# Kernel tuning notes

Measured on AMD Instinct MI355X. Metric: run time of the kernel, lower is better.

The kernel has to match this reference:

```python
import jax, jax.numpy as jnp
import numpy as np

EPS = 1e-5
NHEAD = 8

def layer_norm(x, g, b):
    mu = jnp.mean(x, axis=-1, keepdims=True)
    var = jnp.mean((x - mu) ** 2, axis=-1, keepdims=True)
    return (x - mu) * jax.lax.rsqrt(var + EPS) * g + b

def setup_inputs() -> dict:
    key = jax.random.key(0)
    ks = jax.random.split(key, 8)
    B, S, D, F = 4, 2048, 512, 2048
    s = 0.02
    return {
        "x": jax.random.normal(ks[0], (B, S, D), jnp.float32),
        "Wqkv": jax.random.normal(ks[1], (3 * D, D), jnp.float32) * s,
        "bqkv": jnp.zeros((3 * D,), jnp.float32),
        "Wo": jax.random.normal(ks[2], (D, D), jnp.float32) * s,
        "bo": jnp.zeros((D,), jnp.float32),
        "W1": jax.random.normal(ks[3], (F, D), jnp.float32) * s,
        "b1": jnp.zeros((F,), jnp.float32),
        "W2": jax.random.normal(ks[4], (D, F), jnp.float32) * s,
        "b2": jnp.zeros((D,), jnp.float32),
        "g1": jnp.ones((D,), jnp.float32),
        "bn1": jnp.zeros((D,), jnp.float32),
        "g2": jnp.ones((D,), jnp.float32),
        "bn2": jnp.zeros((D,), jnp.float32),
    }

def reference(x, Wqkv, bqkv, Wo, bo, W1, b1, W2, b2, g1, bn1, g2, bn2):
    B, S, D = x.shape
    H = NHEAD
    hd = D // H
    # fused QKV projection (torch MultiheadAttention in_proj)
    qkv = x @ Wqkv.T + bqkv                      # [B,S,3D]
    q, k, v = jnp.split(qkv, 3, axis=-1)
    q = q.reshape(B, S, H, hd).transpose(0, 2, 1, 3)  # [B,H,S,hd]
    k = k.reshape(B, S, H, hd).transpose(0, 2, 1, 3)
    v = v.reshape(B, S, H, hd).transpose(0, 2, 1, 3)
    scores = jnp.einsum("bhqd,bhkd->bhqk", q, k) / jnp.sqrt(jnp.float32(hd))
    causal = jnp.tril(jnp.ones((S, S), bool))
    scores = jnp.where(causal, scores, jnp.float32(-jnp.inf))
    attn = jax.nn.softmax(scores, axis=-1)
    ctx = jnp.einsum("bhqk,bhkd->bhqd", attn, v)        # [B,H,S,hd]
    ctx = ctx.transpose(0, 2, 1, 3).reshape(B, S, D)
    attn_out = ctx @ Wo.T + bo
    # residual + LayerNorm 1
    x = layer_norm(x + attn_out, g1, bn1)
    # FFN (ReLU) + residual + LayerNorm 2
    ff = jax.nn.relu(x @ W1.T + b1) @ W2.T + b2
    x = layer_norm(x + ff, g2, bn2)
    return x
```

## Files before the change

### kernel.cpp

```cpp
#include <hip/hip_runtime.h>
#include <hip/hip_bf16.h>
#include <math.h>

#define D_MODEL 512
#define SEQ     2048
#define BATCH   4
#define NHEADS  8
#define HDIM    64
#define FFN     2048
#define TOKENS  (BATCH*SEQ)

typedef __attribute__((ext_vector_type(8))) short bf16x8;
typedef __attribute__((ext_vector_type(4))) float f32x4;

__device__ inline ushort f2bf(float f) {
    unsigned u = __builtin_bit_cast(unsigned, f);
    unsigned r = (u + 0x7fffu + ((u >> 16) & 1u)) >> 16;
    return (ushort)r;
}
__device__ inline ushort f2bf_fast(float f) {
    return (ushort)((__builtin_bit_cast(unsigned, f) + 0x8000u) >> 16);
}

#define GLOAD_LDS16(g, l) __builtin_amdgcn_global_load_lds( \
    (const __attribute__((address_space(1))) void*)(g), \
    (__attribute__((address_space(3))) void*)(l), 16, 0, 0)

__global__ void cast_all_bf16(const float* __restrict__ x, const float* __restrict__ Wqkv,
                              const float* __restrict__ Wo, const float* __restrict__ W1,
                              const float* __restrict__ W2, ushort* __restrict__ outbase) {
    const int i = blockIdx.x * blockDim.x + threadIdx.x;
    if (i >= 1835008) return;
    float4 v;
    if      (i < 1048576) v = ((const float4*)x)[i];
    else if (i < 1245184) v = ((const float4*)Wqkv)[i - 1048576];
    else if (i < 1310720) v = ((const float4*)Wo)[i - 1245184];
    else if (i < 1572864) v = ((const float4*)W1)[i - 1310720];
    else                  v = ((const float4*)W2)[i - 1572864];
    ushort4 o;
    o.x = f2bf(v.x); o.y = f2bf(v.y); o.z = f2bf(v.z); o.w = f2bf(v.w);
    ((ushort4*)outbase)[i] = o;
}

template<int MODE, int RELU>
__global__ __launch_bounds__(256) void gemm_bt_mfma(const ushort* __restrict__ A,
                                                    const ushort* __restrict__ W,
                                                    const float* __restrict__ bias,
                                                    void* __restrict__ CoutA,
                                                    void* __restrict__ CoutB,
                                                    ushort* __restrict__ Qc,
                                                    ushort* __restrict__ Kc,
                                                    ushort* __restrict__ Vt,
                                                    int M, int N, int Kstride, int Klen) {
    __shared__ ushort Asb[128 * 32];
    __shared__ ushort Bsb[128 * 32];

    const int tid  = threadIdx.x;
    const int lane = tid & 63;
    const int wv   = tid >> 6;
    const int m0   = blockIdx.y * 128;
    const int n0   = blockIdx.x * 128;
    const int wm   = (wv >> 1) * 64;
    const int wn   = (wv & 1) * 64;
    const int ksel = (MODE == 3) ? blockIdx.z : 0;

    const ushort* Ab = A + (size_t)ksel * Klen;
    const ushort* Wb = W + (size_t)ksel * Klen;

    const int eA = wv * 1024 + lane * 8;
    const int rA = eA >> 5, cA = eA & 31;
    const ushort* gA0 = Ab + (size_t)(m0 + rA) * Kstride + cA;
    const ushort* gA1 = gA0 + (size_t)16 * Kstride;
    const ushort* gB0 = Wb + (size_t)(n0 + rA) * Kstride + cA;
    const ushort* gB1 = gB0 + (size_t)16 * Kstride;
    ushort* lA0 = Asb + wv * 1024;
    ushort* lA1 = Asb + wv * 1024 + 512;
    ushort* lB0 = Bsb + wv * 1024;
    ushort* lB1 = Bsb + wv * 1024 + 512;

    f32x4 acc[4][4] = {};

    const int fr = lane & 15;
    const int fk = (lane >> 4) * 8;

    for (int k0 = 0; k0 < Klen; k0 += 32) {
        GLOAD_LDS16(gA0, lA0); GLOAD_LDS16(gA1, lA1);
        GLOAD_LDS16(gB0, lB0); GLOAD_LDS16(gB1, lB1);
        gA0 += 32; gA1 += 32; gB0 += 32; gB1 += 32;
        __syncthreads();

        bf16x8 af[4], bfr[4];
        #pragma unroll
        for (int i = 0; i < 4; ++i)
            af[i] = *(const bf16x8*)(Asb + (wm + i * 16 + fr) * 32 + fk);
        #pragma unroll
        for (int j = 0; j < 4; ++j)
            bfr[j] = *(const bf16x8*)(Bsb + (wn + j * 16 + fr) * 32 + fk);

        #pragma unroll
        for (int i = 0; i < 4; ++i)
            #pragma unroll
            for (int j = 0; j < 4; ++j)
                acc[i][j] = __builtin_amdgcn_mfma_f32_16x16x32_bf16(af[i], bfr[j], acc[i][j], 0, 0, 0);
        __syncthreads();
    }

    const int col  = lane & 15;
    const int rowq = (lane >> 4) * 4;
    #pragma unroll
    for (int i = 0; i < 4; ++i) {
        const int gm = m0 + wm + i * 16 + rowq;
        #pragma unroll
        for (int j = 0; j < 4; ++j) {
            const int gn = n0 + wn + j * 16 + col;
            if (MODE == 2) {
                const float bv = bias[gn];
                const int seg = gn >> 9;
                const int h   = (gn >> 6) & 7;
                const int dd  = gn & 63;
                const int bb  = gm >> 11;
                const int ss  = gm & 2047;
                const int bh  = bb * 8 + h;
                if (seg == 2) {
                    ushort4 pk;
                    pk.x = f2bf(acc[i][j][0] + bv);
                    pk.y = f2bf(acc[i][j][1] + bv);
                    pk.z = f2bf(acc[i][j][2] + bv);
                    pk.w = f2bf(acc[i][j][3] + bv);
                    *(ushort4*)(Vt + ((size_t)bh * 64 + dd) * 2048 + ss) = pk;
                } else {
                    ushort* dst = (seg == 0 ? Qc : Kc) + ((size_t)bh * 2048 + ss) * 64 + dd;
                    #pragma unroll
                    for (int r = 0; r < 4; ++r)
                        dst[(size_t)r * 64] = f2bf(acc[i][j][r] + bv);
                }
            } else if (MODE == 3) {
                float* dst = (float*)(ksel ? CoutB : CoutA);
                const float bv = ksel ? 0.f : bias[gn];
                #pragma unroll
                for (int r = 0; r < 4; ++r)
                    dst[(size_t)(gm + r) * N + gn] = acc[i][j][r] + bv;
            } else {
                const float bv = bias[gn];
                #pragma unroll
                for (int r = 0; r < 4; ++r) {
                    float v = acc[i][j][r] + bv;
                    if (RELU) v = fmaxf(v, 0.f);
                    ((ushort*)CoutA)[(size_t)(gm + r) * N + gn] = f2bf(v);
                }
            }
        }
    }
}

__device__ __forceinline__ void attn_step(const ushort* __restrict__ Kb,
                                          const ushort* __restrict__ Vb,
                                          ushort* __restrict__ Psw,
                                          bf16x8 qf0, bf16x8 qf1,
                                          float (&lp)[4], f32x4 (&o)[4],
                                          int qw, int j0, bool diag,
                                          int col, int g, int c7) {
    f32x4 s[4] = {};
    #pragma unroll
    for (int nt = 0; nt < 4; ++nt) {
        const int kr = nt * 16 + col;
        bf16x8 kf0 = *(const bf16x8*)(Kb + kr * 64 + (((g    ) ^ c7) * 8));
        bf16x8 kf1 = *(const bf16x8*)(Kb + kr * 64 + (((g + 4) ^ c7) * 8));
        s[nt] = __builtin_amdgcn_mfma_f32_16x16x32_bf16(qf0, kf0, s[nt], 0, 0, 0);
        s[nt] = __builtin_amdgcn_mfma_f32_16x16x32_bf16(qf1, kf1, s[nt], 0, 0, 0);
    }

    if (diag) {
        #pragma unroll
        for (int nt = 0; nt < 4; ++nt)
            #pragma unroll
            for (int r = 0; r < 4; ++r)
                if ((j0 + nt * 16 + col) > (qw + 4 * g + r)) s[nt][r] = -INFINITY;
    }

    #pragma unroll
    for (int nt = 0; nt < 4; ++nt)
        #pragma unroll
        for (int r = 0; r < 4; ++r) {
            float p = __expf(s[nt][r] * 0.125f);
            s[nt][r] = p;
            lp[r] += p;
        }

    #pragma unroll
    for (int nt = 0; nt < 4; ++nt)
        #pragma unroll
        for (int r = 0; r < 4; ++r) {
            const int q  = 4 * g + r;
            const int bc = 32 * nt + 2 * col;
            *(ushort*)((char*)Psw + q * 128 + (((bc >> 4) ^ (q & 7)) * 16) + (bc & 15)) =
                f2bf_fast(s[nt][r]);
        }

    {
        bf16x8 pf0 = *(const bf16x8*)(Psw + col * 64 + (((g    ) ^ c7) * 8));
        bf16x8 pf1 = *(const bf16x8*)(Psw + col * 64 + (((g + 4) ^ c7) * 8));
        #pragma unroll
        for (int nt = 0; nt < 4; ++nt) {
            const int vr = nt * 16 + col;
            bf16x8 vf0 = *(const bf16x8*)(Vb + vr * 64 + (((g    ) ^ c7) * 8));
            bf16x8 vf1 = *(const bf16x8*)(Vb + vr * 64 + (((g + 4) ^ c7) * 8));
            o[nt] = __builtin_amdgcn_mfma_f32_16x16x32_bf16(pf0, vf0, o[nt], 0, 0, 0);
            o[nt] = __builtin_amdgcn_mfma_f32_16x16x32_bf16(pf1, vf1, o[nt], 0, 0, 0);
        }
    }
}

__global__ __launch_bounds__(256) void attn_mfma_kernel(const ushort* __restrict__ Qc,
                                                        const ushort* __restrict__ Kc,
                                                        const ushort* __restrict__ Vt,
                                                        ushort* __restrict__ ctxb) {
    __shared__ ushort Ks[2 * 64 * 64];
    __shared__ ushort Vs[2 * 64 * 64];
    __shared__ ushort Ps[64 * 64];

    const int tid  = threadIdx.x;
    const int lane = tid & 63;
    const int wv   = tid >> 6;
    const int pair = blockIdx.x;
    const int bh   = blockIdx.y;
    const int q0a  = pair * 64;
    const int q0b  = (31 - pair) * 64;
    const int qwA  = q0a + wv * 16;
    const int qwB  = q0b + wv * 16;

    const int col = lane & 15;
    const int g   = lane >> 4;
    const int c7  = col & 7;

    bf16x8 qfA0, qfA1, qfB0, qfB1;
    {
        const ushort* qa = Qc + ((size_t)bh * 2048 + qwA + col) * 64 + g * 8;
        qfA0 = *(const bf16x8*)qa;
        qfA1 = *(const bf16x8*)(qa + 32);
        const ushort* qb = Qc + ((size_t)bh * 2048 + qwB + col) * 64 + g * 8;
        qfB0 = *(const bf16x8*)qb;
        qfB1 = *(const bf16x8*)(qb + 32);
    }

    const int srow = tid >> 2;
    const int sch  = 2 * (tid & 3);
    const ushort* Kg = Kc + ((size_t)bh * 2048 + srow) * 64 + sch * 8;
    const ushort* Vg = Vt + ((size_t)bh * 64 + srow) * 2048 + sch * 8;
    const int ko0 = srow * 64 + (((sch    ) ^ (srow & 7)) * 8);
    const int ko1 = srow * 64 + (((sch + 1) ^ (srow & 7)) * 8);
    ushort* Psw = Ps + wv * 1024;

    float lpa[4] = {}, lpb[4] = {};
    f32x4 oa[4] = {}, ob[4] = {};

    bf16x8 pk0 = *(const bf16x8*)(Kg);
    bf16x8 pk1 = *(const bf16x8*)(Kg + 8);
    bf16x8 pv0 = *(const bf16x8*)(Vg);
    bf16x8 pv1 = *(const bf16x8*)(Vg + 8);

    for (int j0 = 0; j0 <= q0b; j0 += 64) {
        const int par = (j0 >> 6) & 1;
        ushort* Kb = Ks + par * 4096;
        ushort* Vb = Vs + par * 4096;
        *(bf16x8*)(Kb + ko0) = pk0; *(bf16x8*)(Kb + ko1) = pk1;
        *(bf16x8*)(Vb + ko0) = pv0; *(bf16x8*)(Vb + ko1) = pv1;
        __syncthreads();

        if (j0 < q0b) {
            pk0 = *(const bf16x8*)(Kg + (size_t)(j0 + 64) * 64);
            pk1 = *(const bf16x8*)(Kg + (size_t)(j0 + 64) * 64 + 8);
            pv0 = *(const bf16x8*)(Vg + j0 + 64);
            pv1 = *(const bf16x8*)(Vg + j0 + 72);
        }

        if (j0 <= q0a)
            attn_step(Kb, Vb, Psw, qfA0, qfA1, lpa, oa, qwA, j0, j0 == q0a, col, g, c7);
        attn_step(Kb, Vb, Psw, qfB0, qfB1, lpb, ob, qwB, j0, j0 == q0b, col, g, c7);
    }

    const int b = bh >> 3, h = bh & 7;
    #pragma unroll
    for (int r = 0; r < 4; ++r) {
        float la = lpa[r];
        la += __shfl_xor(la, 1); la += __shfl_xor(la, 2);
        la += __shfl_xor(la, 4); la += __shfl_xor(la, 8);
        float lb = lpb[r];
        lb += __shfl_xor(lb, 1); lb += __shfl_xor(lb, 2);
        lb += __shfl_xor(lb, 4); lb += __shfl_xor(lb, 8);
        const float inva = 1.f / la;
        const float invb = 1.f / lb;
        const size_t rowa = ((size_t)b * 2048 + qwA + 4 * g + r) * 512 + h * 64;
        const size_t rowb = ((size_t)b * 2048 + qwB + 4 * g + r) * 512 + h * 64;
        #pragma unroll
        for (int nt = 0; nt < 4; ++nt) {
            ctxb[rowa + nt * 16 + col] = f2bf(oa[nt][r] * inva);
            ctxb[rowb + nt * 16 + col] = f2bf(ob[nt][r] * invb);
        }
    }
}

template<int WRITE_BF16>
__global__ void ln_residual(const float* __restrict__ A, const float* __restrict__ B1,
                            const float* __restrict__ B2,
                            const float* __restrict__ g, const float* __restrict__ beta,
                            float* __restrict__ out, ushort* __restrict__ outb) {
    __shared__ float sbuf[8];
    const int row = blockIdx.x;
    const int tid = threadIdx.x;
    const size_t base = (size_t)row * D_MODEL;

    float v0 = A[base + tid]       + B1[base + tid]       + B2[base + tid];
    float v1 = A[base + tid + 256] + B1[base + tid + 256] + B2[base + tid + 256];

    float sum = v0 + v1;
    #pragma unroll
    for (int off = 32; off; off >>= 1) sum += __shfl_xor(sum, off);
    if ((tid & 63) == 0) sbuf[tid >> 6] = sum;
    __syncthreads();
    if (tid == 0) { float t = 0.f; for (int i = 0; i < 4; ++i) t += sbuf[i]; sbuf[4] = t; }
    __syncthreads();
    const float mu = sbuf[4] * (1.f / 512.f);
    __syncthreads();

    float d0 = v0 - mu, d1 = v1 - mu;
    float sq = d0 * d0 + d1 * d1;
    #pragma unroll
    for (int off = 32; off; off >>= 1) sq += __shfl_xor(sq, off);
    if ((tid & 63) == 0) sbuf[tid >> 6] = sq;
    __syncthreads();
    if (tid == 0) { float t = 0.f; for (int i = 0; i < 4; ++i) t += sbuf[i]; sbuf[4] = t; }
    __syncthreads();
    const float var = sbuf[4] * (1.f / 512.f);
    const float rs  = rsqrtf(var + 1e-5f);

    float r0 = d0 * rs * g[tid]       + beta[tid];
    float r1 = d1 * rs * g[tid + 256] + beta[tid + 256];
    out[base + tid]       = r0;
    out[base + tid + 256] = r1;
    if (WRITE_BF16) {
        outb[base + tid]       = f2bf(r0);
        outb[base + tid + 256] = f2bf(r1);
    }
}

extern "C" void kernel_launch(void* const* d_in, const int* in_sizes, int n_in,
                              void* d_out, int out_size, void* d_ws, size_t ws_size,
                              hipStream_t stream) {
    const float* x    = (const float*)d_in[0];
    const float* Wqkv = (const float*)d_in[1];
    const float* bqkv = (const float*)d_in[2];
    const float* Wo   = (const float*)d_in[3];
    const float* bo   = (const float*)d_in[4];
    const float* W1   = (const float*)d_in[5];
    const float* b1   = (const float*)d_in[6];
    const float* W2   = (const float*)d_in[7];
    const float* b2   = (const float*)d_in[8];
    const float* g1   = (const float*)d_in[9];
    const float* bn1  = (const float*)d_in[10];
    const float* g2   = (const float*)d_in[11];
    const float* bn2  = (const float*)d_in[12];

    float* ws = (float*)d_ws;
    ushort* Qcb     = (ushort*)ws;
    ushort* Kcb     = (ushort*)(ws + 2097152);
    ushort* Vtb     = (ushort*)(ws + 4194304);
    float*  attn_b  = ws;
    ushort* ff1b    = (ushort*)ws;
    float*  ff2a    = ws + 8388608;
    float*  attn_a  = ws + 12582912;
    float*  ff2b    = ws + 12582912;
    float*  ln1     = ws + 16777216;
    ushort* ctxb  = (ushort*)(ws + 20971520);
    ushort* ln1b  = (ushort*)(ws + 23068672);
    ushort* xb    = (ushort*)(ws + 25165824);
    ushort* Wqkvb = (ushort*)(ws + 27262976);
    float*  out   = (float*)d_out;
    ushort* W1b   = (ushort*)(ws + 27787264);
    ushort* W2b   = (ushort*)(ws + 28311552);
    ushort* Wob   = (ushort*)(ws + 27656192);

    const dim3 blk(256);

    cast_all_bf16<<<dim3(7168), blk, 0, stream>>>(x, Wqkv, Wo, W1, W2, xb);

    gemm_bt_mfma<2,0><<<dim3(1536/128, 8192/128), blk, 0, stream>>>(
        xb, Wqkvb, bqkv, nullptr, nullptr, Qcb, Kcb, Vtb, TOKENS, 1536, 512, 512);
    attn_mfma_kernel<<<dim3(16, BATCH*NHEADS), blk, 0, stream>>>(Qcb, Kcb, Vtb, ctxb);
    gemm_bt_mfma<3,0><<<dim3(512/128, 8192/128, 2), blk, 0, stream>>>(
        ctxb, Wob, bo, attn_a, attn_b, nullptr, nullptr, nullptr, TOKENS, 512, 512, 256);
    ln_residual<1><<<dim3(TOKENS), blk, 0, stream>>>(x, attn_a, attn_b, g1, bn1, ln1, ln1b);
    gemm_bt_mfma<1,1><<<dim3(2048/128, 8192/128), blk, 0, stream>>>(
        ln1b, W1b, b1, ff1b, nullptr, nullptr, nullptr, nullptr, TOKENS, 2048, 512, 512);
    gemm_bt_mfma<3,0><<<dim3(512/128, 8192/128, 2), blk, 0, stream>>>(
        ff1b, W2b, b2, ff2a, ff2b, nullptr, nullptr, nullptr, TOKENS, 512, 2048, 1024);
    ln_residual<0><<<dim3(TOKENS), blk, 0, stream>>>(ln1, ff2a, ff2b, g2, bn2, out, nullptr);
}
```

Measured before the change: 269.9 us.

## Split attention key range across two partitions and add a combine kernel

The causal attention kernel now launches a second grid dimension that splits the key tiles between two blocks by even/odd tile index. Each block writes unnormalized fp32 partial outputs and row sums to workspace. A new combine kernel adds the two partials, normalizes, and writes the bf16 context. This doubles the number of blocks to improve latency hiding and CU occupancy, at the cost of extra fp32 partial writes and reads plus one more kernel launch.

```diff
diff --git a/kernel.cpp b/kernel.cpp
--- a/kernel.cpp
+++ b/kernel.cpp
@@ -214,7 +214,8 @@
 __global__ __launch_bounds__(256) void attn_mfma_kernel(const ushort* __restrict__ Qc,
                                                         const ushort* __restrict__ Kc,
                                                         const ushort* __restrict__ Vt,
-                                                        ushort* __restrict__ ctxb) {
+                                                        float* __restrict__ opart,
+                                                        float* __restrict__ lpart) {
     __shared__ ushort Ks[2 * 64 * 64];
     __shared__ ushort Vs[2 * 64 * 64];
     __shared__ ushort Ps[64 * 64];
@@ -224,10 +225,12 @@
     const int wv   = tid >> 6;
     const int pair = blockIdx.x;
     const int bh   = blockIdx.y;
+    const int z    = blockIdx.z;
     const int q0a  = pair * 64;
     const int q0b  = (31 - pair) * 64;
     const int qwA  = q0a + wv * 16;
     const int qwB  = q0b + wv * 16;
+    const int jtmax = 31 - pair;
 
     const int col = lane & 15;
     const int g   = lane >> 4;
@@ -254,24 +257,25 @@
     float lpa[4] = {}, lpb[4] = {};
     f32x4 oa[4] = {}, ob[4] = {};
 
-    bf16x8 pk0 = *(const bf16x8*)(Kg);
-    bf16x8 pk1 = *(const bf16x8*)(Kg + 8);
-    bf16x8 pv0 = *(const bf16x8*)(Vg);
-    bf16x8 pv1 = *(const bf16x8*)(Vg + 8);
-
-    for (int j0 = 0; j0 <= q0b; j0 += 64) {
-        const int par = (j0 >> 6) & 1;
+    bf16x8 pk0 = *(const bf16x8*)(Kg + (size_t)(z << 6) * 64);
+    bf16x8 pk1 = *(const bf16x8*)(Kg + (size_t)(z << 6) * 64 + 8);
+    bf16x8 pv0 = *(const bf16x8*)(Vg + (z << 6));
+    bf16x8 pv1 = *(const bf16x8*)(Vg + (z << 6) + 8);
+
+    for (int jt = z; jt <= jtmax; jt += 2) {
+        const int j0  = jt << 6;
+        const int par = (jt >> 1) & 1;
         ushort* Kb = Ks + par * 4096;
         ushort* Vb = Vs + par * 4096;
         *(bf16x8*)(Kb + ko0) = pk0; *(bf16x8*)(Kb + ko1) = pk1;
         *(bf16x8*)(Vb + ko0) = pv0; *(bf16x8*)(Vb + ko1) = pv1;
         __syncthreads();
 
-        if (j0 < q0b) {
-            pk0 = *(const bf16x8*)(Kg + (size_t)(j0 + 64) * 64);
-            pk1 = *(const bf16x8*)(Kg + (size_t)(j0 + 64) * 64 + 8);
-            pv0 = *(const bf16x8*)(Vg + j0 + 64);
-            pv1 = *(const bf16x8*)(Vg + j0 + 72);
+        if (jt + 2 <= jtmax) {
+            pk0 = *(const bf16x8*)(Kg + (size_t)(j0 + 128) * 64);
+            pk1 = *(const bf16x8*)(Kg + (size_t)(j0 + 128) * 64 + 8);
+            pv0 = *(const bf16x8*)(Vg + j0 + 128);
+            pv1 = *(const bf16x8*)(Vg + j0 + 136);
         }
 
         if (j0 <= q0a)
@@ -280,6 +284,8 @@
     }
 
     const int b = bh >> 3, h = bh & 7;
+    float* od = opart + (size_t)z * 4194304;
+    float* ld = lpart + z * 65536 + bh * 2048;
     #pragma unroll
     for (int r = 0; r < 4; ++r) {
         float la = lpa[r];
@@ -288,16 +294,38 @@
         float lb = lpb[r];
         lb += __shfl_xor(lb, 1); lb += __shfl_xor(lb, 2);
         lb += __shfl_xor(lb, 4); lb += __shfl_xor(lb, 8);
-        const float inva = 1.f / la;
-        const float invb = 1.f / lb;
         const size_t rowa = ((size_t)b * 2048 + qwA + 4 * g + r) * 512 + h * 64;
         const size_t rowb = ((size_t)b * 2048 + qwB + 4 * g + r) * 512 + h * 64;
         #pragma unroll
         for (int nt = 0; nt < 4; ++nt) {
-            ctxb[rowa + nt * 16 + col] = f2bf(oa[nt][r] * inva);
-            ctxb[rowb + nt * 16 + col] = f2bf(ob[nt][r] * invb);
-        }
-    }
+            od[rowa + nt * 16 + col] = oa[nt][r];
+            od[rowb + nt * 16 + col] = ob[nt][r];
+        }
+        if (col == 0) {
+            ld[qwA + 4 * g + r] = la;
+            ld[qwB + 4 * g + r] = lb;
+        }
+    }
+}
+
+__global__ void attn_combine(const float* __restrict__ o0, const float* __restrict__ o1,
+                             const float* __restrict__ l0, const float* __restrict__ l1,
+                             ushort* __restrict__ ctxb) {
+    const int idx = blockIdx.x * 256 + threadIdx.x;
+    const int m  = idx >> 7;
+    const int nq = idx & 127;
+    const int b = m >> 11, s = m & 2047;
+    const int h = nq >> 4;
+    const int li = (b * 8 + h) * 2048 + s;
+    const float inv = 1.f / (l0[li] + l1[li]);
+    float4 a = ((const float4*)o0)[idx];
+    float4 c = ((const float4*)o1)[idx];
+    ushort4 o;
+    o.x = f2bf((a.x + c.x) * inv);
+    o.y = f2bf((a.y + c.y) * inv);
+    o.z = f2bf((a.z + c.z) * inv);
+    o.w = f2bf((a.w + c.w) * inv);
+    ((ushort4*)ctxb)[idx] = o;
 }
 
 template<int WRITE_BF16>
@@ -367,6 +395,8 @@
     ushort* Vtb     = (ushort*)(ws + 4194304);
     float*  attn_b  = ws;
     ushort* ff1b    = (ushort*)ws;
+    float*  opart   = ws + 8388608;
+    float*  lpart   = ws + 16777216;
     float*  ff2a    = ws + 8388608;
     float*  attn_a  = ws + 12582912;
     float*  ff2b    = ws + 12582912;
@@ -386,7 +416,9 @@
 
     gemm_bt_mfma<2,0><<<dim3(1536/128, 8192/128), blk, 0, stream>>>(
         xb, Wqkvb, bqkv, nullptr, nullptr, Qcb, Kcb, Vtb, TOKENS, 1536, 512, 512);
-    attn_mfma_kernel<<<dim3(16, BATCH*NHEADS), blk, 0, stream>>>(Qcb, Kcb, Vtb, ctxb);
+    attn_mfma_kernel<<<dim3(16, BATCH*NHEADS, 2), blk, 0, stream>>>(Qcb, Kcb, Vtb, opart, lpart);
+    attn_combine<<<dim3(4096), blk, 0, stream>>>(opart, opart + 4194304,
+                                                 lpart, lpart + 65536, ctxb);
     gemm_bt_mfma<3,0><<<dim3(512/128, 8192/128, 2), blk, 0, stream>>>(
         ctxb, Wob, bo, attn_a, attn_b, nullptr, nullptr, nullptr, TOKENS, 512, 512, 256);
     ln_residual<1><<<dim3(TOKENS), blk, 0, stream>>>(x, attn_a, attn_b, g1, bn1, ln1, ln1b);
```

Result: slower. 279.1 us (+3.4%).

## Keep attention P in registers via transposed QK^T and permlane swaps

Applied to the files above, without the earlier changes.

The attention step now computes S transposed (K as the A operand) so each lane holds scores for one query column. P is packed to bf16 with v_cvt_pk_bf16_f32 and redistributed with permlane32/permlane16 swaps, which removes the per-wave LDS round trip for P and the Ps shared buffer. Row-sum reduction becomes a single scalar per lane. The grid is flattened to 1D with a batch/head swizzle and launch bounds request 4 blocks per CU. The change relies on gfx950-specific instructions through inline asm, and the operand layout must match exactly for correctness.

```diff
diff --git a/kernel.cpp b/kernel.cpp
--- a/kernel.cpp
+++ b/kernel.cpp
@@ -12,14 +12,12 @@
 
 typedef __attribute__((ext_vector_type(8))) short bf16x8;
 typedef __attribute__((ext_vector_type(4))) float f32x4;
+typedef __attribute__((ext_vector_type(4))) unsigned u32x4;
 
 __device__ inline ushort f2bf(float f) {
     unsigned u = __builtin_bit_cast(unsigned, f);
     unsigned r = (u + 0x7fffu + ((u >> 16) & 1u)) >> 16;
     return (ushort)r;
-}
-__device__ inline ushort f2bf_fast(float f) {
-    return (ushort)((__builtin_bit_cast(unsigned, f) + 0x8000u) >> 16);
 }
 
 #define GLOAD_LDS16(g, l) __builtin_amdgcn_global_load_lds( \
@@ -155,9 +153,8 @@
 
 __device__ __forceinline__ void attn_step(const ushort* __restrict__ Kb,
                                           const ushort* __restrict__ Vb,
-                                          ushort* __restrict__ Psw,
                                           bf16x8 qf0, bf16x8 qf1,
-                                          float (&lp)[4], f32x4 (&o)[4],
+                                          float& lp, f32x4 (&o)[4],
                                           int qw, int j0, bool diag,
                                           int col, int g, int c7) {
     f32x4 s[4] = {};
@@ -166,8 +163,8 @@
         const int kr = nt * 16 + col;
         bf16x8 kf0 = *(const bf16x8*)(Kb + kr * 64 + (((g    ) ^ c7) * 8));
         bf16x8 kf1 = *(const bf16x8*)(Kb + kr * 64 + (((g + 4) ^ c7) * 8));
-        s[nt] = __builtin_amdgcn_mfma_f32_16x16x32_bf16(qf0, kf0, s[nt], 0, 0, 0);
-        s[nt] = __builtin_amdgcn_mfma_f32_16x16x32_bf16(qf1, kf1, s[nt], 0, 0, 0);
+        s[nt] = __builtin_amdgcn_mfma_f32_16x16x32_bf16(kf0, qf0, s[nt], 0, 0, 0);
+        s[nt] = __builtin_amdgcn_mfma_f32_16x16x32_bf16(kf1, qf1, s[nt], 0, 0, 0);
     }
 
     if (diag) {
@@ -175,55 +172,57 @@
         for (int nt = 0; nt < 4; ++nt)
             #pragma unroll
             for (int r = 0; r < 4; ++r)
-                if ((j0 + nt * 16 + col) > (qw + 4 * g + r)) s[nt][r] = -INFINITY;
-    }
-
-    #pragma unroll
-    for (int nt = 0; nt < 4; ++nt)
-        #pragma unroll
-        for (int r = 0; r < 4; ++r) {
-            float p = __expf(s[nt][r] * 0.125f);
-            s[nt][r] = p;
-            lp[r] += p;
-        }
-
-    #pragma unroll
-    for (int nt = 0; nt < 4; ++nt)
-        #pragma unroll
-        for (int r = 0; r < 4; ++r) {
-            const int q  = 4 * g + r;
-            const int bc = 32 * nt + 2 * col;
-            *(ushort*)((char*)Psw + q * 128 + (((bc >> 4) ^ (q & 7)) * 16) + (bc & 15)) =
-                f2bf_fast(s[nt][r]);
-        }
-
-    {
-        bf16x8 pf0 = *(const bf16x8*)(Psw + col * 64 + (((g    ) ^ c7) * 8));
-        bf16x8 pf1 = *(const bf16x8*)(Psw + col * 64 + (((g + 4) ^ c7) * 8));
-        #pragma unroll
-        for (int nt = 0; nt < 4; ++nt) {
-            const int vr = nt * 16 + col;
-            bf16x8 vf0 = *(const bf16x8*)(Vb + vr * 64 + (((g    ) ^ c7) * 8));
-            bf16x8 vf1 = *(const bf16x8*)(Vb + vr * 64 + (((g + 4) ^ c7) * 8));
-            o[nt] = __builtin_amdgcn_mfma_f32_16x16x32_bf16(pf0, vf0, o[nt], 0, 0, 0);
-            o[nt] = __builtin_amdgcn_mfma_f32_16x16x32_bf16(pf1, vf1, o[nt], 0, 0, 0);
-        }
-    }
-}
-
-__global__ __launch_bounds__(256) void attn_mfma_kernel(const ushort* __restrict__ Qc,
-                                                        const ushort* __restrict__ Kc,
-                                                        const ushort* __restrict__ Vt,
-                                                        ushort* __restrict__ ctxb) {
+                if ((j0 + nt * 16 + 4 * g + r) > (qw + col)) s[nt][r] = -INFINITY;
+    }
+
+    unsigned W[8];
+    #pragma unroll
+    for (int nt = 0; nt < 4; ++nt) {
+        float p0 = __expf(s[nt][0] * 0.125f);
+        float p1 = __expf(s[nt][1] * 0.125f);
+        float p2 = __expf(s[nt][2] * 0.125f);
+        float p3 = __expf(s[nt][3] * 0.125f);
+        lp += (p0 + p1) + (p2 + p3);
+        asm("v_cvt_pk_bf16_f32 %0, %1, %2" : "=v"(W[2 * nt])     : "v"(p0), "v"(p1));
+        asm("v_cvt_pk_bf16_f32 %0, %1, %2" : "=v"(W[2 * nt + 1]) : "v"(p2), "v"(p3));
+    }
+    asm("v_permlane32_swap_b32 %0, %1" : "+v"(W[0]), "+v"(W[2]));
+    asm("v_permlane32_swap_b32 %0, %1" : "+v"(W[1]), "+v"(W[3]));
+    asm("v_permlane32_swap_b32 %0, %1" : "+v"(W[4]), "+v"(W[6]));
+    asm("v_permlane32_swap_b32 %0, %1" : "+v"(W[5]), "+v"(W[7]));
+    asm("v_permlane16_swap_b32 %0, %1" : "+v"(W[0]), "+v"(W[2]));
+    asm("v_permlane16_swap_b32 %0, %1" : "+v"(W[1]), "+v"(W[3]));
+    asm("v_permlane16_swap_b32 %0, %1" : "+v"(W[4]), "+v"(W[6]));
+    asm("v_permlane16_swap_b32 %0, %1" : "+v"(W[5]), "+v"(W[7]));
+
+    u32x4 wa = {W[0], W[1], W[2], W[3]};
+    u32x4 wb = {W[4], W[5], W[6], W[7]};
+    bf16x8 pf0 = __builtin_bit_cast(bf16x8, wa);
+    bf16x8 pf1 = __builtin_bit_cast(bf16x8, wb);
+
+    #pragma unroll
+    for (int nt = 0; nt < 4; ++nt) {
+        const int vr = nt * 16 + col;
+        bf16x8 vf0 = *(const bf16x8*)(Vb + vr * 64 + (((g    ) ^ c7) * 8));
+        bf16x8 vf1 = *(const bf16x8*)(Vb + vr * 64 + (((g + 4) ^ c7) * 8));
+        o[nt] = __builtin_amdgcn_mfma_f32_16x16x32_bf16(pf0, vf0, o[nt], 0, 0, 0);
+        o[nt] = __builtin_amdgcn_mfma_f32_16x16x32_bf16(pf1, vf1, o[nt], 0, 0, 0);
+    }
+}
+
+__global__ __launch_bounds__(256, 4) void attn_mfma_kernel(const ushort* __restrict__ Qc,
+                                                           const ushort* __restrict__ Kc,
+                                                           const ushort* __restrict__ Vt,
+                                                           ushort* __restrict__ ctxb) {
     __shared__ ushort Ks[2 * 64 * 64];
     __shared__ ushort Vs[2 * 64 * 64];
-    __shared__ ushort Ps[64 * 64];
 
     const int tid  = threadIdx.x;
     const int lane = tid & 63;
     const int wv   = tid >> 6;
-    const int pair = blockIdx.x;
-    const int bh   = blockIdx.y;
+    const int idx  = blockIdx.x;
+    const int bh   = (idx & 7) * 4 + (idx >> 7);
+    const int pair = (idx >> 3) & 15;
     const int q0a  = pair * 64;
     const int q0b  = (31 - pair) * 64;
     const int qwA  = q0a + wv * 16;
@@ -249,9 +248,8 @@
     const ushort* Vg = Vt + ((size_t)bh * 64 + srow) * 2048 + sch * 8;
     const int ko0 = srow * 64 + (((sch    ) ^ (srow & 7)) * 8);
     const int ko1 = srow * 64 + (((sch + 1) ^ (srow & 7)) * 8);
-    ushort* Psw = Ps + wv * 1024;
-
-    float lpa[4] = {}, lpb[4] = {};
+
+    float lpa = 0.f, lpb = 0.f;
     f32x4 oa[4] = {}, ob[4] = {};
 
     bf16x8 pk0 = *(const bf16x8*)(Kg);
@@ -275,21 +273,17 @@
         }
 
         if (j0 <= q0a)
-            attn_step(Kb, Vb, Psw, qfA0, qfA1, lpa, oa, qwA, j0, j0 == q0a, col, g, c7);
-        attn_step(Kb, Vb, Psw, qfB0, qfB1, lpb, ob, qwB, j0, j0 == q0b, col, g, c7);
-    }
-
+            attn_step(Kb, Vb, qfA0, qfA1, lpa, oa, qwA, j0, j0 == q0a, col, g, c7);
+        attn_step(Kb, Vb, qfB0, qfB1, lpb, ob, qwB, j0, j0 == q0b, col, g, c7);
+    }
+
+    float la = lpa; la += __shfl_xor(la, 16); la += __shfl_xor(la, 32);
+    float lb = lpb; lb += __shfl_xor(lb, 16); lb += __shfl_xor(lb, 32);
     const int b = bh >> 3, h = bh & 7;
     #pragma unroll
     for (int r = 0; r < 4; ++r) {
-        float la = lpa[r];
-        la += __shfl_xor(la, 1); la += __shfl_xor(la, 2);
-        la += __shfl_xor(la, 4); la += __shfl_xor(la, 8);
-        float lb = lpb[r];
-        lb += __shfl_xor(lb, 1); lb += __shfl_xor(lb, 2);
-        lb += __shfl_xor(lb, 4); lb += __shfl_xor(lb, 8);
-        const float inva = 1.f / la;
-        const float invb = 1.f / lb;
+        const float inva = 1.f / __shfl(la, 4 * g + r);
+        const float invb = 1.f / __shfl(lb, 4 * g + r);
         const size_t rowa = ((size_t)b * 2048 + qwA + 4 * g + r) * 512 + h * 64;
         const size_t rowb = ((size_t)b * 2048 + qwB + 4 * g + r) * 512 + h * 64;
         #pragma unroll
@@ -386,7 +380,7 @@
 
     gemm_bt_mfma<2,0><<<dim3(1536/128, 8192/128), blk, 0, stream>>>(
         xb, Wqkvb, bqkv, nullptr, nullptr, Qcb, Kcb, Vtb, TOKENS, 1536, 512, 512);
-    attn_mfma_kernel<<<dim3(16, BATCH*NHEADS), blk, 0, stream>>>(Qcb, Kcb, Vtb, ctxb);
+    attn_mfma_kernel<<<dim3(512), blk, 0, stream>>>(Qcb, Kcb, Vtb, ctxb);
     gemm_bt_mfma<3,0><<<dim3(512/128, 8192/128, 2), blk, 0, stream>>>(
         ctxb, Wob, bo, attn_a, attn_b, nullptr, nullptr, nullptr, TOKENS, 512, 512, 256);
     ln_residual<1><<<dim3(TOKENS), blk, 0, stream>>>(x, attn_a, attn_b, g1, bn1, ln1, ln1b);
```

Measured after the change: 265.0 us. About the same (-1.8%).
